# Kernel optimization log

Measured on AMD Instinct MI355X. Metric: run time of the kernel, lower is better.

The kernel has to match this reference:

```python
import jax, jax.numpy as jnp
import numpy as np

N_NODES = 100000

def _gcn_norm(edge_index, num_nodes):
    # add self-loops, compute symmetric normalization coeffs per edge
    loops = jnp.arange(num_nodes, dtype=edge_index.dtype)
    src = jnp.concatenate([edge_index[0], loops])
    dst = jnp.concatenate([edge_index[1], loops])
    deg = jax.ops.segment_sum(jnp.ones_like(dst, dtype=jnp.float32), dst,
                              num_segments=num_nodes)
    dinv = jnp.where(deg > 0, jax.lax.rsqrt(deg), 0.0)
    norm = dinv[src] * dinv[dst]  # [E + N]
    return src, dst, norm

def _gcn_conv(x, W, b, src, dst, norm, num_nodes):
    h = x @ W                              # [N, out] transform first (PyG order)
    msg = h[src] * norm[:, None]           # gather + scale
    out = jax.ops.segment_sum(msg, dst, num_segments=num_nodes)  # scatter-add
    return out + b

def setup_inputs() -> dict:
    key = jax.random.key(0)
    k1, k2, k3, k4 = jax.random.split(key, 4)
    F_in, H, C = 128, 64, 40
    x = jax.random.normal(k1, (N_NODES, F_in), dtype=jnp.float32)
    edge_index = jax.random.randint(k2, (2, 1600000), 0, N_NODES, dtype=jnp.int64)
    W1 = jax.random.normal(k3, (F_in, H), dtype=jnp.float32) / np.sqrt(F_in)
    b1 = jnp.zeros((H,), dtype=jnp.float32)
    W2 = jax.random.normal(k4, (H, C), dtype=jnp.float32) / np.sqrt(H)
    b2 = jnp.zeros((C,), dtype=jnp.float32)
    return {"x": x, "edge_index": edge_index, "W1": W1, "b1": b1, "W2": W2, "b2": b2}

def reference(x, edge_index, W1, b1, W2, b2):
    num_nodes = x.shape[0]
    src, dst, norm = _gcn_norm(edge_index, num_nodes)
    h = _gcn_conv(x, W1, b1, src, dst, norm, num_nodes)
    h = jax.nn.relu(h)
    # dropout is identity in eval mode (training=False)
    h = _gcn_conv(h, W2, b2, src, dst, norm, num_nodes)
    return jax.nn.log_softmax(h, axis=1)
```

## Files before the change

### kernel.cpp

```cpp
#include <hip/hip_runtime.h>
#include <math.h>

#define NPB 256
#define BSH 8
#define MAXNB 400
#define BIN_CHUNK 8192
#define HIST_CHUNK 16384

typedef __attribute__((ext_vector_type(8))) short bf16x8;
typedef __attribute__((ext_vector_type(4))) float f32x4;
typedef __attribute__((ext_vector_type(2))) float f32x2;

__device__ __forceinline__ unsigned short f2bf(float f){
  unsigned int u = __float_as_uint(f);
  unsigned int r = (u + 0x7FFFu + ((u >> 16) & 1u)) >> 16;
  return (unsigned short)r;
}
__device__ __forceinline__ float bf2f(unsigned int b){
  return __uint_as_float(b << 16);
}


__global__ void k_zero(int* __restrict__ p, int n){
  int i = blockIdx.x*256 + threadIdx.x;
  if(i < n) p[i] = 0;
}

__global__ __launch_bounds__(256) void k_bhist(const int* __restrict__ dst, int E,
                                               int* __restrict__ bcnt, int NB){
  __shared__ int l[MAXNB];
  int t = threadIdx.x;
  int base = blockIdx.x*HIST_CHUNK;
  int end = base + HIST_CHUNK; if(end > E) end = E;
  for(int b = t; b < NB; b += 256) l[b] = 0;
  __syncthreads();
  for(int i = base + t; i < end; i += 256) atomicAdd(&l[dst[i] >> BSH], 1);
  __syncthreads();
  for(int b = t; b < NB; b += 256){ int c = l[b]; if(c) atomicAdd(&bcnt[b], c); }
}

__global__ void k_bscan(const int* __restrict__ bcnt, int* __restrict__ bofs,
                        int* __restrict__ bcur, int NB, int E){
  __shared__ int sh[1024];
  int t = threadIdx.x;
  int c0 = (2*t   < NB) ? bcnt[2*t]   : 0;
  int c1 = (2*t+1 < NB) ? bcnt[2*t+1] : 0;
  sh[t] = c0 + c1; __syncthreads();
  for(int off = 1; off < 1024; off <<= 1){
    int v = (t >= off) ? sh[t - off] : 0;
    __syncthreads();
    sh[t] += v;
    __syncthreads();
  }
  int pairEx = sh[t] - (c0 + c1);
  if(2*t   < NB){ bofs[2*t]   = pairEx;      bcur[2*t]   = pairEx; }
  if(2*t+1 < NB){ bofs[2*t+1] = pairEx + c0; bcur[2*t+1] = pairEx + c0; }
  if(t == 0) bofs[NB] = E;
}

__global__ __launch_bounds__(256) void k_binpass(const int* __restrict__ src,
                          const int* __restrict__ dst, int E,
                          int* __restrict__ bcur, unsigned int* __restrict__ binned, int NB){
  __shared__ int lcnt[MAXNB];
  __shared__ int lpos[MAXNB];
  int t = threadIdx.x;
  int base = blockIdx.x * BIN_CHUNK;
  int end = base + BIN_CHUNK; if(end > E) end = E;
  for(int b = t; b < NB; b += 256) lcnt[b] = 0;
  __syncthreads();
  for(int i = base + t; i < end; i += 256)
    atomicAdd(&lcnt[dst[i] >> BSH], 1);
  __syncthreads();
  for(int b = t; b < NB; b += 256){
    int c = lcnt[b];
    lpos[b] = c ? atomicAdd(&bcur[b], c) : 0;
  }
  __syncthreads();
  for(int i = base + t; i < end; i += 256){
    int d = dst[i];
    int b = d >> BSH;
    unsigned int rec = (unsigned int)src[i] | ((unsigned int)(d & (NPB-1)) << 17);
    int p = atomicAdd(&lpos[b], 1);
    binned[p] = rec;
  }
}

__global__ __launch_bounds__(256) void k_bscatter(const unsigned int* __restrict__ binned,
     const int* __restrict__ bofs, int* __restrict__ csr, int* __restrict__ row_ofs,
     float* __restrict__ dinv, int N, int E, int NB){
  __shared__ int lcnt[NPB];
  __shared__ int lofs[NPB];
  __shared__ int lcur[NPB];
  __shared__ int wsum[4];
  int b = blockIdx.x, t = threadIdx.x;
  int beg = bofs[b], end = bofs[b+1];
  lcnt[t] = 0;
  __syncthreads();
  for(int i = beg + t; i < end; i += 256) atomicAdd(&lcnt[binned[i] >> 17], 1);
  __syncthreads();
  int c = lcnt[t];
  int lane = t & 63, wid = t >> 6;
  int v = c;
  #pragma unroll
  for(int off = 1; off < 64; off <<= 1){
    int nv = __shfl_up(v, off, 64);
    if(lane >= off) v += nv;
  }
  if(lane == 63) wsum[wid] = v;
  __syncthreads();
  int wpre = 0;
  #pragma unroll
  for(int k2 = 0; k2 < 4; k2++) if(k2 < wid) wpre += wsum[k2];
  int ex = wpre + v - c;
  lofs[t] = beg + ex; lcur[t] = 0;
  int node = (b << BSH) + t;
  if(node < N){
    row_ofs[node] = beg + ex;
    dinv[node] = rsqrtf((float)(c + 1));
  }
  __syncthreads();
  for(int i = beg + t; i < end; i += 256){
    unsigned int rec = binned[i];
    int dl = rec >> 17;
    int pos = lofs[dl] + atomicAdd(&lcur[dl], 1);
    csr[pos] = (int)(rec & 0x1FFFFu);
  }
  if(b == NB-1 && t == 0) row_ofs[N] = E;
}

__global__ __launch_bounds__(256) void k_gemm1(const float* __restrict__ x, const float* __restrict__ W1,
                        const float* __restrict__ dinv, unsigned int* __restrict__ g1, int n){
  __shared__ unsigned short xs[64*136];
  __shared__ unsigned short wt[64*136];
  int tid = threadIdx.x;
  int nodeBase = blockIdx.x*64;
  {
    const float4* x4 = (const float4*)x;
    for(int i = tid; i < 2048; i += 256){
      int node = i >> 5, kg = i & 31;
      float4 v = make_float4(0.f,0.f,0.f,0.f);
      if(nodeBase + node < n) v = x4[(size_t)(nodeBase + node)*32 + kg];
      unsigned p0 = (unsigned)f2bf(v.x) | ((unsigned)f2bf(v.y) << 16);
      unsigned p1 = (unsigned)f2bf(v.z) | ((unsigned)f2bf(v.w) << 16);
      *(uint2*)&xs[node*136 + kg*4] = make_uint2(p0, p1);
    }
  }
  {
    for(int i = tid; i < 2048; i += 256){
      int nn = i >> 5, kq = i & 31;
      unsigned short q0 = f2bf(W1[(kq*4+0)*64 + nn]);
      unsigned short q1 = f2bf(W1[(kq*4+1)*64 + nn]);
      unsigned short q2 = f2bf(W1[(kq*4+2)*64 + nn]);
      unsigned short q3 = f2bf(W1[(kq*4+3)*64 + nn]);
      unsigned p0 = (unsigned)q0 | ((unsigned)q1 << 16);
      unsigned p1 = (unsigned)q2 | ((unsigned)q3 << 16);
      *(uint2*)&wt[nn*136 + kq*4] = make_uint2(p0, p1);
    }
  }
  __syncthreads();

  int w = tid >> 6, lane = tid & 63;
  int ml = lane & 15, q = lane >> 4;
  f32x4 acc0 = {0.f,0.f,0.f,0.f}, acc1 = {0.f,0.f,0.f,0.f},
        acc2 = {0.f,0.f,0.f,0.f}, acc3 = {0.f,0.f,0.f,0.f};
  const unsigned short* brow = &xs[(w*16 + ml)*136 + q*8];
  const unsigned short* arow = &wt[ml*136 + q*8];
  #pragma unroll
  for(int s = 0; s < 4; s++){
    bf16x8 bb = *(const bf16x8*)(brow + s*32);
    bf16x8 a0 = *(const bf16x8*)(arow +   0*136 + s*32);
    bf16x8 a1 = *(const bf16x8*)(arow +  16*136 + s*32);
    bf16x8 a2 = *(const bf16x8*)(arow +  32*136 + s*32);
    bf16x8 a3 = *(const bf16x8*)(arow +  48*136 + s*32);
    acc0 = __builtin_amdgcn_mfma_f32_16x16x32_bf16(a0, bb, acc0, 0, 0, 0);
    acc1 = __builtin_amdgcn_mfma_f32_16x16x32_bf16(a1, bb, acc1, 0, 0, 0);
    acc2 = __builtin_amdgcn_mfma_f32_16x16x32_bf16(a2, bb, acc2, 0, 0, 0);
    acc3 = __builtin_amdgcn_mfma_f32_16x16x32_bf16(a3, bb, acc3, 0, 0, 0);
  }
  int node = nodeBase + w*16 + ml;
  if(node < n){
    float dv = dinv[node];
    unsigned base16 = ((unsigned)node << 4) + q;
    int p;
    p = __builtin_amdgcn_cvt_pk_fp8_f32(acc0[0]*dv, acc0[1]*dv, 0, false);
    p = __builtin_amdgcn_cvt_pk_fp8_f32(acc0[2]*dv, acc0[3]*dv, p, true);
    g1[base16 +  0] = (unsigned)p;
    p = __builtin_amdgcn_cvt_pk_fp8_f32(acc1[0]*dv, acc1[1]*dv, 0, false);
    p = __builtin_amdgcn_cvt_pk_fp8_f32(acc1[2]*dv, acc1[3]*dv, p, true);
    g1[base16 +  4] = (unsigned)p;
    p = __builtin_amdgcn_cvt_pk_fp8_f32(acc2[0]*dv, acc2[1]*dv, 0, false);
    p = __builtin_amdgcn_cvt_pk_fp8_f32(acc2[2]*dv, acc2[3]*dv, p, true);
    g1[base16 +  8] = (unsigned)p;
    p = __builtin_amdgcn_cvt_pk_fp8_f32(acc3[0]*dv, acc3[1]*dv, 0, false);
    p = __builtin_amdgcn_cvt_pk_fp8_f32(acc3[2]*dv, acc3[3]*dv, p, true);
    g1[base16 + 12] = (unsigned)p;
  }
}

__global__ __launch_bounds__(256) void k_agg1(const unsigned* __restrict__ g1,
    const int* __restrict__ row_ofs, const int* __restrict__ csr,
    const float* __restrict__ dinv, const float* __restrict__ b1,
    unsigned short* __restrict__ u, int N){
  int t = threadIdx.x;
  int lane = t & 63;
  int f = lane & 15;
  int bq = (lane & 48) << 2;
  int node = blockIdx.x*16 + (t >> 4);
  if(node >= N) return;
  int beg = row_ofs[node], end = row_ofs[node+1];
  unsigned v = g1[((unsigned)node << 4) + f];
  f32x2 s01 = __builtin_amdgcn_cvt_pk_f32_fp8(v, false);
  f32x2 s23 = __builtin_amdgcn_cvt_pk_f32_fp8(v, true);
  for(int e = beg; e < end; e += 16){
    int rem = end - e; if(rem > 16) rem = 16;
    int idxv = (f < rem) ? csr[e + f] : 0;
    int j = 0;
    for(; j + 4 <= rem; j += 4){
      int r0 = __builtin_amdgcn_ds_bpermute(bq + ((j+0) << 2), idxv);
      int r1 = __builtin_amdgcn_ds_bpermute(bq + ((j+1) << 2), idxv);
      int r2 = __builtin_amdgcn_ds_bpermute(bq + ((j+2) << 2), idxv);
      int r3 = __builtin_amdgcn_ds_bpermute(bq + ((j+3) << 2), idxv);
      unsigned v0 = g1[((unsigned)r0 << 4) + f];
      unsigned v1 = g1[((unsigned)r1 << 4) + f];
      unsigned v2 = g1[((unsigned)r2 << 4) + f];
      unsigned v3 = g1[((unsigned)r3 << 4) + f];
      s01 += __builtin_amdgcn_cvt_pk_f32_fp8(v0, false);
      s23 += __builtin_amdgcn_cvt_pk_f32_fp8(v0, true);
      s01 += __builtin_amdgcn_cvt_pk_f32_fp8(v1, false);
      s23 += __builtin_amdgcn_cvt_pk_f32_fp8(v1, true);
      s01 += __builtin_amdgcn_cvt_pk_f32_fp8(v2, false);
      s23 += __builtin_amdgcn_cvt_pk_f32_fp8(v2, true);
      s01 += __builtin_amdgcn_cvt_pk_f32_fp8(v3, false);
      s23 += __builtin_amdgcn_cvt_pk_f32_fp8(v3, true);
    }
    for(; j < rem; j++){
      int r0 = __builtin_amdgcn_ds_bpermute(bq + (j << 2), idxv);
      unsigned v0 = g1[((unsigned)r0 << 4) + f];
      s01 += __builtin_amdgcn_cvt_pk_f32_fp8(v0, false);
      s23 += __builtin_amdgcn_cvt_pk_f32_fp8(v0, true);
    }
  }
  float dv = dinv[node];
  float4 bb = ((const float4*)b1)[f];
  float h0 = fmaxf(fmaf(dv, s01.x, bb.x), 0.f);
  float h1 = fmaxf(fmaf(dv, s01.y, bb.y), 0.f);
  float h2 = fmaxf(fmaf(dv, s23.x, bb.z), 0.f);
  float h3 = fmaxf(fmaf(dv, s23.y, bb.w), 0.f);
  unsigned p0 = (unsigned)f2bf(dv*h0) | ((unsigned)f2bf(dv*h1) << 16);
  unsigned p1 = (unsigned)f2bf(dv*h2) | ((unsigned)f2bf(dv*h3) << 16);
  ((uint2*)u)[((unsigned)node << 4) + f] = make_uint2(p0, p1);
}

__global__ __launch_bounds__(320) void k_gemm2(const unsigned short* __restrict__ u,
                        const float* __restrict__ W2, unsigned char* __restrict__ g2, int n){
  __shared__ float hs[64*65];
  __shared__ float ws[64*40];
  int t = threadIdx.x;
  int nodeBase = blockIdx.x*64;
  for(int i = t; i < 2560; i += 320) ws[i] = W2[i];
  for(int i = t; i < 512; i += 320){
    int row = i >> 3, seg = i & 7;
    uint4 v = make_uint4(0,0,0,0);
    if(nodeBase + row < n) v = *(const uint4*)&u[(size_t)(nodeBase + row)*64 + seg*8];
    float* dp = &hs[row*65 + seg*8];
    dp[0]=bf2f(v.x&0xFFFFu); dp[1]=bf2f(v.x>>16);
    dp[2]=bf2f(v.y&0xFFFFu); dp[3]=bf2f(v.y>>16);
    dp[4]=bf2f(v.z&0xFFFFu); dp[5]=bf2f(v.z>>16);
    dp[6]=bf2f(v.w&0xFFFFu); dp[7]=bf2f(v.w>>16);
  }
  __syncthreads();
  int seg = t >> 6, lane = t & 63;
  float acc[8] = {0.f,0.f,0.f,0.f,0.f,0.f,0.f,0.f};
  const float* hrow = &hs[lane*65];
  const float* wcol = &ws[seg*8];
  #pragma unroll 4
  for(int k = 0; k < 64; k++){
    float a = hrow[k];
    #pragma unroll
    for(int j = 0; j < 8; j++) acc[j] = fmaf(a, wcol[k*40 + j], acc[j]);
  }
  int node = nodeBase + lane;
  if(node < n){
    int p0 = __builtin_amdgcn_cvt_pk_fp8_f32(acc[0], acc[1], 0, false);
    p0     = __builtin_amdgcn_cvt_pk_fp8_f32(acc[2], acc[3], p0, true);
    int p1 = __builtin_amdgcn_cvt_pk_fp8_f32(acc[4], acc[5], 0, false);
    p1     = __builtin_amdgcn_cvt_pk_fp8_f32(acc[6], acc[7], p1, true);
    *(uint2*)&g2[(size_t)node*40 + seg*8] = make_uint2((unsigned)p0, (unsigned)p1);
  }
}

__global__ __launch_bounds__(256) void k_agg2(const unsigned char* __restrict__ g2,
     const int* __restrict__ row_ofs, const int* __restrict__ csr,
     const float* __restrict__ dinv, const float* __restrict__ b2,
     float* __restrict__ out, int N){
  int t = threadIdx.x;
  int lane = t & 63;
  int f = lane & 15;
  int fc = (f < 10) ? f : 0;
  int bq = (lane & 48) << 2;
  int node = blockIdx.x*16 + (t >> 4);
  if(node >= N) return;
  int beg = row_ofs[node], end = row_ofs[node+1];
  const unsigned* gd = (const unsigned*)g2;
  unsigned v = gd[(unsigned)node*10u + fc];
  f32x2 s01 = __builtin_amdgcn_cvt_pk_f32_fp8(v, false);
  f32x2 s23 = __builtin_amdgcn_cvt_pk_f32_fp8(v, true);
  for(int e = beg; e < end; e += 16){
    int rem = end - e; if(rem > 16) rem = 16;
    int idxv = (f < rem) ? csr[e + f] : 0;
    int j = 0;
    for(; j + 4 <= rem; j += 4){
      int r0 = __builtin_amdgcn_ds_bpermute(bq + ((j+0) << 2), idxv);
      int r1 = __builtin_amdgcn_ds_bpermute(bq + ((j+1) << 2), idxv);
      int r2 = __builtin_amdgcn_ds_bpermute(bq + ((j+2) << 2), idxv);
      int r3 = __builtin_amdgcn_ds_bpermute(bq + ((j+3) << 2), idxv);
      unsigned v0 = gd[(unsigned)r0*10u + fc];
      unsigned v1 = gd[(unsigned)r1*10u + fc];
      unsigned v2 = gd[(unsigned)r2*10u + fc];
      unsigned v3 = gd[(unsigned)r3*10u + fc];
      s01 += __builtin_amdgcn_cvt_pk_f32_fp8(v0, false);
      s23 += __builtin_amdgcn_cvt_pk_f32_fp8(v0, true);
      s01 += __builtin_amdgcn_cvt_pk_f32_fp8(v1, false);
      s23 += __builtin_amdgcn_cvt_pk_f32_fp8(v1, true);
      s01 += __builtin_amdgcn_cvt_pk_f32_fp8(v2, false);
      s23 += __builtin_amdgcn_cvt_pk_f32_fp8(v2, true);
      s01 += __builtin_amdgcn_cvt_pk_f32_fp8(v3, false);
      s23 += __builtin_amdgcn_cvt_pk_f32_fp8(v3, true);
    }
    for(; j < rem; j++){
      int r0 = __builtin_amdgcn_ds_bpermute(bq + (j << 2), idxv);
      unsigned v0 = gd[(unsigned)r0*10u + fc];
      s01 += __builtin_amdgcn_cvt_pk_f32_fp8(v0, false);
      s23 += __builtin_amdgcn_cvt_pk_f32_fp8(v0, true);
    }
  }
  float dv = dinv[node];
  float4 bb = ((const float4*)b2)[fc];
  float l0 = fmaf(dv, s01.x, bb.x);
  float l1 = fmaf(dv, s01.y, bb.y);
  float l2 = fmaf(dv, s23.x, bb.z);
  float l3 = fmaf(dv, s23.y, bb.w);
  bool valid = (f < 10);
  float m = valid ? fmaxf(fmaxf(l0,l1), fmaxf(l2,l3)) : -INFINITY;
  m = fmaxf(m, __shfl_xor(m,1,64)); m = fmaxf(m, __shfl_xor(m,2,64));
  m = fmaxf(m, __shfl_xor(m,4,64)); m = fmaxf(m, __shfl_xor(m,8,64));
  float ex = valid ? (expf(l0-m)+expf(l1-m)) + (expf(l2-m)+expf(l3-m)) : 0.f;
  ex += __shfl_xor(ex,1,64); ex += __shfl_xor(ex,2,64);
  ex += __shfl_xor(ex,4,64); ex += __shfl_xor(ex,8,64);
  float ll = logf(ex);
  if(valid){
    ((float4*)out)[(unsigned)node*10u + f] = make_float4(l0-m-ll, l1-m-ll, l2-m-ll, l3-m-ll);
  }
}


extern "C" void kernel_launch(void* const* d_in, const int* in_sizes, int n_in,
                              void* d_out, int out_size, void* d_ws, size_t ws_size,
                              hipStream_t stream){
  const float* x  = (const float*)d_in[0];
  const int*   ei = (const int*)  d_in[1];
  const float* W1 = (const float*)d_in[2];
  const float* b1 = (const float*)d_in[3];
  const float* W2 = (const float*)d_in[4];
  const float* b2 = (const float*)d_in[5];
  float* out = (float*)d_out;

  int N = in_sizes[0] / 128;
  int E = in_sizes[1] / 2;
  const int* src = ei;
  const int* dst = ei + E;
  int NB = (N + NPB - 1) >> BSH;

  char* w = (char*)d_ws;
  auto alloc = [&](size_t bytes) -> char* {
    char* p = w;
    w += (bytes + 511) & ~(size_t)511;
    return p;
  };
  int*   bcnt    = (int*)  alloc((size_t)NB*4);
  int*   bofs    = (int*)  alloc((size_t)(NB+1)*4);
  int*   bcur    = (int*)  alloc((size_t)NB*4);
  int*   row_ofs = (int*)  alloc((size_t)(N+1)*4);
  float* dinv    = (float*)alloc((size_t)N*4);
  unsigned int* binned = (unsigned int*)alloc((size_t)E*4);
  int*   csr     = (int*)  alloc((size_t)E*4);
  unsigned int*   g1 = (unsigned int*)  alloc((size_t)N*64);
  unsigned short* u  = (unsigned short*)alloc((size_t)N*64*2);
  unsigned char*  g2 = (unsigned char*) alloc((size_t)N*40);

  k_zero    <<<(NB+255)/256, 256, 0, stream>>>(bcnt, NB);
  k_bhist   <<<(E+HIST_CHUNK-1)/HIST_CHUNK, 256, 0, stream>>>(dst, E, bcnt, NB);
  k_bscan   <<<1, 1024, 0, stream>>>(bcnt, bofs, bcur, NB, E);
  k_binpass <<<(E+BIN_CHUNK-1)/BIN_CHUNK, 256, 0, stream>>>(src, dst, E, bcur, binned, NB);
  k_bscatter<<<NB, 256, 0, stream>>>(binned, bofs, csr, row_ofs, dinv, N, E, NB);

  k_gemm1   <<<(N+63)/64, 256, 0, stream>>>(x, W1, dinv, g1, N);
  k_agg1    <<<(N+15)/16, 256, 0, stream>>>(g1, row_ofs, csr, dinv, b1, u, N);
  k_gemm2   <<<(N+63)/64, 320, 0, stream>>>(u, W2, g2, N);
  k_agg2    <<<(N+15)/16, 256, 0, stream>>>(g2, row_ofs, csr, dinv, b2, out, N);
}
```

Baseline: 261.9 us.

## Pretranspose W1 once and load x directly into MFMA registers in gemm1

Adds a one-block kernel that converts W1 to a transposed bf16 layout once, so each gemm1 block just copies it into shared memory instead of redoing strided conversion. gemm1 now reads x rows straight from global memory into registers, using packed bf16 conversion, and skips the x shared-memory staging. Each wave covers 32 nodes (128 per block), so each W fragment feeds two MFMA tiles. This trims LDS traffic and per-block setup work, at the cost of more accumulator registers, an extra small launch, and less coalesced direct x loads.

Result: no change. 261.5 us (-0.2%).

```diff
diff --git a/kernel.cpp b/kernel.cpp
--- a/kernel.cpp
+++ b/kernel.cpp
@@ -18,6 +18,15 @@
 }
 __device__ __forceinline__ float bf2f(unsigned int b){
   return __uint_as_float(b << 16);
+}
+
+__device__ __forceinline__ bf16x8 cvt8(float4 a, float4 b){
+  union { unsigned u[4]; bf16x8 v; } r;
+  asm("v_cvt_pk_bf16_f32 %0, %1, %2" : "=v"(r.u[0]) : "v"(a.x), "v"(a.y));
+  asm("v_cvt_pk_bf16_f32 %0, %1, %2" : "=v"(r.u[1]) : "v"(a.z), "v"(a.w));
+  asm("v_cvt_pk_bf16_f32 %0, %1, %2" : "=v"(r.u[2]) : "v"(b.x), "v"(b.y));
+  asm("v_cvt_pk_bf16_f32 %0, %1, %2" : "=v"(r.u[3]) : "v"(b.z), "v"(b.w));
+  return r.v;
 }
 
 
@@ -128,71 +137,94 @@
   if(b == NB-1 && t == 0) row_ofs[N] = E;
 }
 
-__global__ __launch_bounds__(256) void k_gemm1(const float* __restrict__ x, const float* __restrict__ W1,
+__global__ void k_wprep(const float* __restrict__ W1, unsigned short* __restrict__ w1t){
+  int t = threadIdx.x;
+  for(int i = t; i < 8192; i += 256){
+    int k = i >> 6, f = i & 63;
+    w1t[f*128 + k] = f2bf(W1[i]);
+  }
+}
+
+__global__ __launch_bounds__(256) void k_gemm1(const float* __restrict__ x,
+                        const unsigned short* __restrict__ w1t,
                         const float* __restrict__ dinv, unsigned int* __restrict__ g1, int n){
-  __shared__ unsigned short xs[64*136];
   __shared__ unsigned short wt[64*136];
   int tid = threadIdx.x;
-  int nodeBase = blockIdx.x*64;
-  {
-    const float4* x4 = (const float4*)x;
-    for(int i = tid; i < 2048; i += 256){
-      int node = i >> 5, kg = i & 31;
-      float4 v = make_float4(0.f,0.f,0.f,0.f);
-      if(nodeBase + node < n) v = x4[(size_t)(nodeBase + node)*32 + kg];
-      unsigned p0 = (unsigned)f2bf(v.x) | ((unsigned)f2bf(v.y) << 16);
-      unsigned p1 = (unsigned)f2bf(v.z) | ((unsigned)f2bf(v.w) << 16);
-      *(uint2*)&xs[node*136 + kg*4] = make_uint2(p0, p1);
-    }
-  }
-  {
-    for(int i = tid; i < 2048; i += 256){
-      int nn = i >> 5, kq = i & 31;
-      unsigned short q0 = f2bf(W1[(kq*4+0)*64 + nn]);
-      unsigned short q1 = f2bf(W1[(kq*4+1)*64 + nn]);
-      unsigned short q2 = f2bf(W1[(kq*4+2)*64 + nn]);
-      unsigned short q3 = f2bf(W1[(kq*4+3)*64 + nn]);
-      unsigned p0 = (unsigned)q0 | ((unsigned)q1 << 16);
-      unsigned p1 = (unsigned)q2 | ((unsigned)q3 << 16);
-      *(uint2*)&wt[nn*136 + kq*4] = make_uint2(p0, p1);
-    }
+  int nodeBase = blockIdx.x*128;
+  for(int i = tid; i < 1024; i += 256){
+    int f = i >> 4, seg = i & 15;
+    uint4 v = *(const uint4*)&w1t[f*128 + seg*8];
+    *(uint4*)&wt[f*136 + seg*8] = v;
   }
   __syncthreads();
 
   int w = tid >> 6, lane = tid & 63;
   int ml = lane & 15, q = lane >> 4;
-  f32x4 acc0 = {0.f,0.f,0.f,0.f}, acc1 = {0.f,0.f,0.f,0.f},
-        acc2 = {0.f,0.f,0.f,0.f}, acc3 = {0.f,0.f,0.f,0.f};
-  const unsigned short* brow = &xs[(w*16 + ml)*136 + q*8];
+  int n0 = nodeBase + w*32 + ml;
+  int n1 = n0 + 16;
+  bool vn0 = n0 < n, vn1 = n1 < n;
+  const float* px0 = x + (size_t)n0*128 + q*8;
+  const float* px1 = x + (size_t)n1*128 + q*8;
+  const float4 z4 = make_float4(0.f,0.f,0.f,0.f);
+
+  f32x4 a00 = {0.f,0.f,0.f,0.f}, a01 = {0.f,0.f,0.f,0.f},
+        a02 = {0.f,0.f,0.f,0.f}, a03 = {0.f,0.f,0.f,0.f};
+  f32x4 a10 = {0.f,0.f,0.f,0.f}, a11 = {0.f,0.f,0.f,0.f},
+        a12 = {0.f,0.f,0.f,0.f}, a13 = {0.f,0.f,0.f,0.f};
   const unsigned short* arow = &wt[ml*136 + q*8];
   #pragma unroll
   for(int s = 0; s < 4; s++){
-    bf16x8 bb = *(const bf16x8*)(brow + s*32);
-    bf16x8 a0 = *(const bf16x8*)(arow +   0*136 + s*32);
-    bf16x8 a1 = *(const bf16x8*)(arow +  16*136 + s*32);
-    bf16x8 a2 = *(const bf16x8*)(arow +  32*136 + s*32);
-    bf16x8 a3 = *(const bf16x8*)(arow +  48*136 + s*32);
-    acc0 = __builtin_amdgcn_mfma_f32_16x16x32_bf16(a0, bb, acc0, 0, 0, 0);
-    acc1 = __builtin_amdgcn_mfma_f32_16x16x32_bf16(a1, bb, acc1, 0, 0, 0);
-    acc2 = __builtin_amdgcn_mfma_f32_16x16x32_bf16(a2, bb, acc2, 0, 0, 0);
-    acc3 = __builtin_amdgcn_mfma_f32_16x16x32_bf16(a3, bb, acc3, 0, 0, 0);
-  }
-  int node = nodeBase + w*16 + ml;
-  if(node < n){
-    float dv = dinv[node];
-    unsigned base16 = ((unsigned)node << 4) + q;
+    float4 xa0 = vn0 ? *(const float4*)(px0 + s*32)     : z4;
+    float4 xb0 = vn0 ? *(const float4*)(px0 + s*32 + 4) : z4;
+    float4 xa1 = vn1 ? *(const float4*)(px1 + s*32)     : z4;
+    float4 xb1 = vn1 ? *(const float4*)(px1 + s*32 + 4) : z4;
+    bf16x8 bb0 = cvt8(xa0, xb0);
+    bf16x8 bb1 = cvt8(xa1, xb1);
+    bf16x8 a0 = *(const bf16x8*)(arow +    0 + s*32);
+    bf16x8 a1 = *(const bf16x8*)(arow + 2176 + s*32);
+    bf16x8 a2 = *(const bf16x8*)(arow + 4352 + s*32);
+    bf16x8 a3 = *(const bf16x8*)(arow + 6528 + s*32);
+    a00 = __builtin_amdgcn_mfma_f32_16x16x32_bf16(a0, bb0, a00, 0, 0, 0);
+    a01 = __builtin_amdgcn_mfma_f32_16x16x32_bf16(a1, bb0, a01, 0, 0, 0);
+    a02 = __builtin_amdgcn_mfma_f32_16x16x32_bf16(a2, bb0, a02, 0, 0, 0);
+    a03 = __builtin_amdgcn_mfma_f32_16x16x32_bf16(a3, bb0, a03, 0, 0, 0);
+    a10 = __builtin_amdgcn_mfma_f32_16x16x32_bf16(a0, bb1, a10, 0, 0, 0);
+    a11 = __builtin_amdgcn_mfma_f32_16x16x32_bf16(a1, bb1, a11, 0, 0, 0);
+    a12 = __builtin_amdgcn_mfma_f32_16x16x32_bf16(a2, bb1, a12, 0, 0, 0);
+    a13 = __builtin_amdgcn_mfma_f32_16x16x32_bf16(a3, bb1, a13, 0, 0, 0);
+  }
+  if(vn0){
+    float dv = dinv[n0];
+    unsigned base16 = ((unsigned)n0 << 4) + q;
     int p;
-    p = __builtin_amdgcn_cvt_pk_fp8_f32(acc0[0]*dv, acc0[1]*dv, 0, false);
-    p = __builtin_amdgcn_cvt_pk_fp8_f32(acc0[2]*dv, acc0[3]*dv, p, true);
+    p = __builtin_amdgcn_cvt_pk_fp8_f32(a00[0]*dv, a00[1]*dv, 0, false);
+    p = __builtin_amdgcn_cvt_pk_fp8_f32(a00[2]*dv, a00[3]*dv, p, true);
     g1[base16 +  0] = (unsigned)p;
-    p = __builtin_amdgcn_cvt_pk_fp8_f32(acc1[0]*dv, acc1[1]*dv, 0, false);
-    p = __builtin_amdgcn_cvt_pk_fp8_f32(acc1[2]*dv, acc1[3]*dv, p, true);
+    p = __builtin_amdgcn_cvt_pk_fp8_f32(a01[0]*dv, a01[1]*dv, 0, false);
+    p = __builtin_amdgcn_cvt_pk_fp8_f32(a01[2]*dv, a01[3]*dv, p, true);
     g1[base16 +  4] = (unsigned)p;
-    p = __builtin_amdgcn_cvt_pk_fp8_f32(acc2[0]*dv, acc2[1]*dv, 0, false);
-    p = __builtin_amdgcn_cvt_pk_fp8_f32(acc2[2]*dv, acc2[3]*dv, p, true);
+    p = __builtin_amdgcn_cvt_pk_fp8_f32(a02[0]*dv, a02[1]*dv, 0, false);
+    p = __builtin_amdgcn_cvt_pk_fp8_f32(a02[2]*dv, a02[3]*dv, p, true);
     g1[base16 +  8] = (unsigned)p;
-    p = __builtin_amdgcn_cvt_pk_fp8_f32(acc3[0]*dv, acc3[1]*dv, 0, false);
-    p = __builtin_amdgcn_cvt_pk_fp8_f32(acc3[2]*dv, acc3[3]*dv, p, true);
+    p = __builtin_amdgcn_cvt_pk_fp8_f32(a03[0]*dv, a03[1]*dv, 0, false);
+    p = __builtin_amdgcn_cvt_pk_fp8_f32(a03[2]*dv, a03[3]*dv, p, true);
+    g1[base16 + 12] = (unsigned)p;
+  }
+  if(vn1){
+    float dv = dinv[n1];
+    unsigned base16 = ((unsigned)n1 << 4) + q;
+    int p;
+    p = __builtin_amdgcn_cvt_pk_fp8_f32(a10[0]*dv, a10[1]*dv, 0, false);
+    p = __builtin_amdgcn_cvt_pk_fp8_f32(a10[2]*dv, a10[3]*dv, p, true);
+    g1[base16 +  0] = (unsigned)p;
+    p = __builtin_amdgcn_cvt_pk_fp8_f32(a11[0]*dv, a11[1]*dv, 0, false);
+    p = __builtin_amdgcn_cvt_pk_fp8_f32(a11[2]*dv, a11[3]*dv, p, true);
+    g1[base16 +  4] = (unsigned)p;
+    p = __builtin_amdgcn_cvt_pk_fp8_f32(a12[0]*dv, a12[1]*dv, 0, false);
+    p = __builtin_amdgcn_cvt_pk_fp8_f32(a12[2]*dv, a12[3]*dv, p, true);
+    g1[base16 +  8] = (unsigned)p;
+    p = __builtin_amdgcn_cvt_pk_fp8_f32(a13[0]*dv, a13[1]*dv, 0, false);
+    p = __builtin_amdgcn_cvt_pk_fp8_f32(a13[2]*dv, a13[3]*dv, p, true);
     g1[base16 + 12] = (unsigned)p;
   }
 }
@@ -387,14 +419,16 @@
   unsigned int*   g1 = (unsigned int*)  alloc((size_t)N*64);
   unsigned short* u  = (unsigned short*)alloc((size_t)N*64*2);
   unsigned char*  g2 = (unsigned char*) alloc((size_t)N*40);
-
+  unsigned short* w1t = (unsigned short*)alloc((size_t)64*128*2);
+
+  k_wprep   <<<1, 256, 0, stream>>>(W1, w1t);
   k_zero    <<<(NB+255)/256, 256, 0, stream>>>(bcnt, NB);
   k_bhist   <<<(E+HIST_CHUNK-1)/HIST_CHUNK, 256, 0, stream>>>(dst, E, bcnt, NB);
   k_bscan   <<<1, 1024, 0, stream>>>(bcnt, bofs, bcur, NB, E);
   k_binpass <<<(E+BIN_CHUNK-1)/BIN_CHUNK, 256, 0, stream>>>(src, dst, E, bcur, binned, NB);
   k_bscatter<<<NB, 256, 0, stream>>>(binned, bofs, csr, row_ofs, dinv, N, E, NB);
 
-  k_gemm1   <<<(N+63)/64, 256, 0, stream>>>(x, W1, dinv, g1, N);
+  k_gemm1   <<<(N+127)/128, 256, 0, stream>>>(x, w1t, dinv, g1, N);
   k_agg1    <<<(N+15)/16, 256, 0, stream>>>(g1, row_ofs, csr, dinv, b1, u, N);
   k_gemm2   <<<(N+63)/64, 320, 0, stream>>>(u, W2, g2, N);
   k_agg2    <<<(N+15)/16, 256, 0, stream>>>(g2, row_ofs, csr, dinv, b2, out, N);
```
